# Kernel tuning notes

Hardware: AMD Instinct MI355X
Metric: run time of the kernel (lower is better)

## Reference

```python
import jax, jax.numpy as jnp
import numpy as np

IN_F, OUT_F, M, BATCH = 64, 64, 20, 1024


def setup_inputs() -> dict:
    key = jax.random.key(0)
    k1, k2 = jax.random.split(key)
    x = jax.random.normal(k1, (BATCH, IN_F), dtype=jnp.float32)
    # parameters, initialized as in the torch module
    z = jnp.tile(jnp.linspace(-1.5, 1.5, M, dtype=jnp.float32).reshape(1, 1, M), (OUT_F, IN_F, 1))
    q_mu = jax.random.normal(k2, (OUT_F, IN_F, M), dtype=jnp.float32) * 0.05
    q_log_var = jnp.full((OUT_F, IN_F, M), -3.0, dtype=jnp.float32)
    log_scale = jnp.zeros((OUT_F, IN_F), dtype=jnp.float32)
    log_variance = jnp.full((OUT_F, IN_F), -1.0, dtype=jnp.float32)
    return {"x": x, "z": z, "q_mu": q_mu, "q_log_var": q_log_var,
            "log_scale": log_scale, "log_variance": log_variance}


def reference(x, z, q_mu, q_log_var, log_scale, log_variance):
    """SVGP-KAN layer, RBF kernel, deterministic input path (x_var = 1e-6).

    Per edge (o,i): basis-function GP f(x) = sum_m w_m k(x, z_m),
    w_m ~ N(q_mu, q_var), k(x,z) = sig2 * exp(-(x-z)^2 / (2 l^2)).
    Gaussian input x ~ N(mu, v) -> closed-form moments (Psi statistics).
    """
    x_mean = x
    x_var = jnp.full_like(x, 1e-6)

    q_var = jnp.clip(jnp.exp(q_log_var), 1e-5)          # [O,I,M]
    sig2 = jnp.clip(jnp.exp(log_variance), 1e-5)        # [O,I]
    ell = jnp.clip(jnp.exp(log_scale), 0.1)             # [O,I] (rbf min_scale=0.1)

    # broadcast: batch x out x in x inducing
    xm = x_mean[:, None, :, None]                       # [B,1,I,1]
    xv = x_var[:, None, :, None]                        # [B,1,I,1]
    zz = z[None]                                        # [1,O,I,M]
    l2 = (ell * ell)[None, :, :, None]                  # [1,O,I,1]
    s2 = sig2[None, :, :, None]                         # [1,O,I,1]

    d2 = (xm - zz) ** 2                                 # [B,O,I,M]
    den1 = l2 + xv
    psi1 = s2 * jnp.sqrt(l2 / den1) * jnp.exp(-d2 / (2.0 * den1))  # E[k(x,z_m)]
    den2 = l2 + 2.0 * xv
    ek2 = (s2 * s2) * jnp.sqrt(l2 / den2) * jnp.exp(-d2 / den2)     # E[k(x,z_m)^2]

    qm = q_mu[None]                                     # [1,O,I,M]
    qv = q_var[None]
    edge_mean = jnp.sum(psi1 * qm, axis=-1)             # [B,O,I]
    edge_var = jnp.sum(ek2 * (qm * qm + qv) - psi1 * psi1 * (qm * qm), axis=-1)
    edge_var = jnp.clip(edge_var, 0.0)                  # [B,O,I]

    y_mean = edge_mean.sum(axis=2)                      # [B,O]
    y_var = edge_var.sum(axis=2)                        # [B,O]
    return y_mean, y_var
```

## Files before the change

kernel.cpp:

```cpp
#include <hip/hip_runtime.h>
#include <hip/hip_bf16.h>

#define OUT_F 64
#define IN_F 64
#define M_PTS 20
#define BATCH 1024

#if __has_builtin(__builtin_amdgcn_exp2f)
#define EXP2(x) __builtin_amdgcn_exp2f(x)
#else
#define EXP2(x) exp2f(x)
#endif

__device__ unsigned g_cp[OUT_F * M_PTS * IN_F];
__device__ float4   g_aux[OUT_F * IN_F];

static __device__ __forceinline__ unsigned f2bf(float f) {
    union { float f; unsigned u; } v; v.f = f;
    unsigned r = v.u + 0x7fffu + ((v.u >> 16) & 1u);
    return r >> 16;
}
static __device__ __forceinline__ float bflo(unsigned p) {
    union { unsigned u; float f; } v; v.u = p << 16; return v.f;
}
static __device__ __forceinline__ float bfhi(unsigned p) {
    union { unsigned u; float f; } v; v.u = p & 0xffff0000u; return v.f;
}

__global__ __launch_bounds__(256) void prep_kernel(
    const float* __restrict__ z, const float* __restrict__ q_mu,
    const float* __restrict__ q_log_var, const float* __restrict__ log_scale,
    const float* __restrict__ log_variance)
{
    int idx = blockIdx.x * 256 + threadIdx.x;
    if (idx >= OUT_F * M_PTS * IN_F) return;
    int i  = idx & 63;
    int om = idx >> 6;
    int m  = om % M_PTS;
    int o  = om / M_PTS;
    int e  = o * IN_F + i;
    int ge = e * M_PTS + m;

    const float LOG2E = 1.4426950408889634f;
    float ell  = fmaxf(expf(log_scale[e]), 0.1f);
    float l2   = ell * ell;
    float sig2 = fmaxf(expf(log_variance[e]), 1e-5f);
    float den1 = l2 + 1e-6f;
    float den2 = l2 + 2e-6f;
    float c1   = sig2 * sqrtf(l2 / den1);
    float c2   = sig2 * sig2 * sqrtf(l2 / den2);
    float s    = sqrtf(0.5f * LOG2E / den1);

    float qm  = q_mu[ge];
    float qv  = fmaxf(expf(q_log_var[ge]), 1e-5f);
    float qmc = c1 * qm;
    float A   = c2 * (qm * qm + qv);
    float B   = A - qmc * qmc;

    g_cp[idx] = f2bf(qmc) | (f2bf(B) << 16);
    if (m == 0) {
        float z0  = z[ge];
        float z19 = z[e * M_PTS + (M_PTS - 1)];
        float delta = (z19 - z0) * (1.0f / (M_PTS - 1));
        float sd = s * delta;
        g_aux[e] = make_float4(s, s * z0, 2.0f * sd, -(sd * sd));
    }
}

__global__ __launch_bounds__(256, 8) void gpkan_main(
    const float* __restrict__ x, float* __restrict__ out)
{
    __shared__ float  xs_lds[8 * 64];
    __shared__ float2 red[4][8][66];

    const int tid  = threadIdx.x;
    const int lane = tid & 63;
    const int wv   = __builtin_amdgcn_readfirstlane(tid >> 6);
    const int o    = blockIdx.y * 4 + wv;
    const int bc   = blockIdx.x;

    if (tid < 128)
        reinterpret_cast<float4*>(xs_lds)[tid] =
            reinterpret_cast<const float4*>(x + bc * 8 * IN_F)[tid];

    float4 aux = g_aux[(o << 6) + lane];
    const float s = aux.x, sz0 = aux.y, cu1 = aux.z, cu0 = aux.w;
    const float v = EXP2(cu0 + cu0);

    unsigned cp[M_PTS];
    #pragma unroll
    for (int m = 0; m < M_PTS; ++m)
        cp[m] = g_cp[((o * M_PTS + m) << 6) + lane];

    __syncthreads();

    #pragma unroll 1
    for (int p = 0; p < 4; ++p) {
        float xb0 = xs_lds[(p << 7) + lane];
        float xb1 = xs_lds[(p << 7) + 64 + lane];
        float dx0 = fmaf(s, xb0, -sz0);
        float dx1 = fmaf(s, xb1, -sz0);
        float t0  = EXP2(-(dx0 * dx0));
        float t1  = EXP2(-(dx1 * dx1));
        float ua0 = fminf(fmaf(cu1, dx0, cu0), 60.0f);
        float ua1 = fminf(fmaf(cu1, dx1, cu0), 60.0f);
        float w0  = EXP2(ua0);
        float w1  = EXP2(ua1);

        float em0 = 0.0f, em1 = 0.0f, ev0 = 0.0f, ev1 = 0.0f;
        #pragma unroll
        for (int m = 0; m < M_PTS; ++m) {
            unsigned c = cp[m];
            float qmc = bflo(c);
            float B   = bfhi(c);
            em0 = fmaf(qmc, t0, em0);
            em1 = fmaf(qmc, t1, em1);
            ev0 = fmaf(B, t0 * t0, ev0);
            ev1 = fmaf(B, t1 * t1, ev1);
            if (m < M_PTS - 1) { t0 *= w0; t1 *= w1; w0 *= v; w1 *= v; }
        }
        red[wv][2 * p + 0][lane] = make_float2(em0, fmaxf(ev0, 0.0f));
        red[wv][2 * p + 1][lane] = make_float2(em1, fmaxf(ev1, 0.0f));
    }
    __syncthreads();

    const int seg = lane >> 3, b8r = lane & 7;
    const float4* rp = reinterpret_cast<const float4*>(&red[wv][b8r][seg << 3]);
    float sm = 0.0f, sv = 0.0f;
    #pragma unroll
    for (int j = 0; j < 4; ++j) {
        float4 q = rp[j];
        sm += q.x + q.z;
        sv += q.y + q.w;
    }
    sm += __shfl_xor(sm, 8);  sv += __shfl_xor(sv, 8);
    sm += __shfl_xor(sm, 16); sv += __shfl_xor(sv, 16);
    sm += __shfl_xor(sm, 32); sv += __shfl_xor(sv, 32);

    if (lane < 8) {
        int b = (bc << 3) + lane;
        out[(b << 6) + o] = sm;
        out[(BATCH << 6) + (b << 6) + o] = sv;
    }
}

extern "C" void kernel_launch(void* const* d_in, const int* in_sizes, int n_in,
                              void* d_out, int out_size, void* d_ws, size_t ws_size,
                              hipStream_t stream) {
    const float* x            = (const float*)d_in[0];
    const float* z            = (const float*)d_in[1];
    const float* q_mu         = (const float*)d_in[2];
    const float* q_log_var    = (const float*)d_in[3];
    const float* log_scale    = (const float*)d_in[4];
    const float* log_variance = (const float*)d_in[5];
    float* out = (float*)d_out;

    prep_kernel<<<(OUT_F * M_PTS * IN_F + 255) / 256, 256, 0, stream>>>(
        z, q_mu, q_log_var, log_scale, log_variance);
    gpkan_main<<<dim3(BATCH / 8, OUT_F / 4), 256, 0, stream>>>(x, out);
}
```

Before: 21.99 us.

## Use single-wave blocks with shuffle-based transpose reduction instead of LDS

Changes the main kernel from 256-thread blocks (4 waves sharing an LDS-staged x tile) to 64-thread single-wave blocks that read x directly from global memory. The LDS reduction buffer and both __syncthreads are replaced by a recursive-halving shuffle reduction that sums 16 values across lanes. The batch loop is fully unrolled through a macro. The aim is to drop barrier and LDS overhead and expose more ILP. The cost is more blocks, redundant global x loads per wave, and higher register pressure from the unrolled body.

Measured after the change: 22.88 us. +4.1%, slower.

```diff
diff --git a/kernel.cpp b/kernel.cpp
--- a/kernel.cpp
+++ b/kernel.cpp
@@ -67,21 +67,41 @@
     }
 }
 
-__global__ __launch_bounds__(256, 8) void gpkan_main(
+#define BODY(P)                                                              \
+    {                                                                        \
+        float xb0 = xg[((2 * (P)) << 6) + lane];                             \
+        float xb1 = xg[((2 * (P) + 1) << 6) + lane];                         \
+        float dx0 = fmaf(s, xb0, -sz0);                                      \
+        float dx1 = fmaf(s, xb1, -sz0);                                      \
+        float t0  = EXP2(-(dx0 * dx0));                                      \
+        float t1  = EXP2(-(dx1 * dx1));                                      \
+        float w0  = EXP2(fminf(fmaf(cu1, dx0, cu0), 60.0f));                 \
+        float w1  = EXP2(fminf(fmaf(cu1, dx1, cu0), 60.0f));                 \
+        float em0 = 0.0f, em1 = 0.0f, ev0 = 0.0f, ev1 = 0.0f;                \
+        _Pragma("unroll")                                                    \
+        for (int m = 0; m < M_PTS; ++m) {                                    \
+            unsigned c = cp[m];                                              \
+            float qmc = bflo(c);                                             \
+            float B   = bfhi(c);                                             \
+            em0 = fmaf(qmc, t0, em0);                                        \
+            em1 = fmaf(qmc, t1, em1);                                        \
+            ev0 = fmaf(B, t0 * t0, ev0);                                     \
+            ev1 = fmaf(B, t1 * t1, ev1);                                     \
+            if (m < M_PTS - 1) { t0 *= w0; t1 *= w1; w0 *= v; w1 *= v; }     \
+        }                                                                    \
+        qa[2 * (P)]     = em0;                                               \
+        qa[2 * (P) + 1] = em1;                                               \
+        qa[8 + 2 * (P)] = fmaxf(ev0, 0.0f);                                  \
+        qa[9 + 2 * (P)] = fmaxf(ev1, 0.0f);                                  \
+    }
+
+__global__ __launch_bounds__(64, 8) void gpkan_main(
     const float* __restrict__ x, float* __restrict__ out)
 {
-    __shared__ float  xs_lds[8 * 64];
-    __shared__ float2 red[4][8][66];
-
-    const int tid  = threadIdx.x;
-    const int lane = tid & 63;
-    const int wv   = __builtin_amdgcn_readfirstlane(tid >> 6);
-    const int o    = blockIdx.y * 4 + wv;
-    const int bc   = blockIdx.x;
-
-    if (tid < 128)
-        reinterpret_cast<float4*>(xs_lds)[tid] =
-            reinterpret_cast<const float4*>(x + bc * 8 * IN_F)[tid];
+    const int blk  = blockIdx.x;
+    const int o    = blk >> 7;
+    const int bc   = blk & 127;
+    const int lane = threadIdx.x;
 
     float4 aux = g_aux[(o << 6) + lane];
     const float s = aux.x, sz0 = aux.y, cu1 = aux.z, cu0 = aux.w;
@@ -92,55 +112,51 @@
     for (int m = 0; m < M_PTS; ++m)
         cp[m] = g_cp[((o * M_PTS + m) << 6) + lane];
 
-    __syncthreads();
+    const float* __restrict__ xg = x + (bc << 9);
 
-    #pragma unroll 1
-    for (int p = 0; p < 4; ++p) {
-        float xb0 = xs_lds[(p << 7) + lane];
-        float xb1 = xs_lds[(p << 7) + 64 + lane];
-        float dx0 = fmaf(s, xb0, -sz0);
-        float dx1 = fmaf(s, xb1, -sz0);
-        float t0  = EXP2(-(dx0 * dx0));
-        float t1  = EXP2(-(dx1 * dx1));
-        float ua0 = fminf(fmaf(cu1, dx0, cu0), 60.0f);
-        float ua1 = fminf(fmaf(cu1, dx1, cu0), 60.0f);
-        float w0  = EXP2(ua0);
-        float w1  = EXP2(ua1);
+    float qa[16];
+    BODY(0) BODY(1) BODY(2) BODY(3)
 
-        float em0 = 0.0f, em1 = 0.0f, ev0 = 0.0f, ev1 = 0.0f;
-        #pragma unroll
-        for (int m = 0; m < M_PTS; ++m) {
-            unsigned c = cp[m];
-            float qmc = bflo(c);
-            float B   = bfhi(c);
-            em0 = fmaf(qmc, t0, em0);
-            em1 = fmaf(qmc, t1, em1);
-            ev0 = fmaf(B, t0 * t0, ev0);
-            ev1 = fmaf(B, t1 * t1, ev1);
-            if (m < M_PTS - 1) { t0 *= w0; t1 *= w1; w0 *= v; w1 *= v; }
-        }
-        red[wv][2 * p + 0][lane] = make_float2(em0, fmaxf(ev0, 0.0f));
-        red[wv][2 * p + 1][lane] = make_float2(em1, fmaxf(ev1, 0.0f));
+    const bool s5 = (lane & 32) != 0;
+    const bool s4 = (lane & 16) != 0;
+    const bool s3 = (lane & 8) != 0;
+    const bool s2 = (lane & 4) != 0;
+
+    float k8[8];
+    #pragma unroll
+    for (int j = 0; j < 8; ++j) {
+        float keep = s5 ? qa[j + 8] : qa[j];
+        float send = s5 ? qa[j] : qa[j + 8];
+        k8[j] = keep + __shfl_xor(send, 32);
     }
-    __syncthreads();
-
-    const int seg = lane >> 3, b8r = lane & 7;
-    const float4* rp = reinterpret_cast<const float4*>(&red[wv][b8r][seg << 3]);
-    float sm = 0.0f, sv = 0.0f;
+    float k4[4];
     #pragma unroll
     for (int j = 0; j < 4; ++j) {
-        float4 q = rp[j];
-        sm += q.x + q.z;
-        sv += q.y + q.w;
+        float keep = s4 ? k8[j + 4] : k8[j];
+        float send = s4 ? k8[j] : k8[j + 4];
+        k4[j] = keep + __shfl_xor(send, 16);
     }
-    sm += __shfl_xor(sm, 8);  sv += __shfl_xor(sv, 8);
-    sm += __shfl_xor(sm, 16); sv += __shfl_xor(sv, 16);
-    sm += __shfl_xor(sm, 32); sv += __shfl_xor(sv, 32);
+    float k2[2];
+    #pragma unroll
+    for (int j = 0; j < 2; ++j) {
+        float keep = s3 ? k4[j + 2] : k4[j];
+        float send = s3 ? k4[j] : k4[j + 2];
+        k2[j] = keep + __shfl_xor(send, 8);
+    }
+    float k1;
+    {
+        float keep = s2 ? k2[1] : k2[0];
+        float send = s2 ? k2[0] : k2[1];
+        k1 = keep + __shfl_xor(send, 4);
+    }
+    k1 += __shfl_xor(k1, 2);
+    k1 += __shfl_xor(k1, 1);
 
-    if (lane < 8) {
-        int b = (bc << 3) + lane;
-        out[(b << 6) + o] = sm;
-        out[(BATCH << 6) + (b << 6) + o] = sv;
+    if ((lane & 3) == 0) {
+        int row   = ((lane >> 4) & 1) * 4 + ((lane >> 3) & 1) * 2 + ((lane >> 2) & 1);
+        int is_ev = (lane >> 5) & 1;
+        int b     = (bc << 3) + row;
+        out[is_ev * (BATCH * OUT_F) + b * OUT_F + o] = k1;
     }
 }
 
@@ -157,5 +173,5 @@
 
     prep_kernel<<<(OUT_F * M_PTS * IN_F + 255) / 256, 256, 0, stream>>>(
         z, q_mu, q_log_var, log_scale, log_variance);
-    gpkan_main<<<dim3(BATCH / 8, OUT_F / 4), 256, 0, stream>>>(x, out);
+    gpkan_main<<<128 * OUT_F, 64, 0, stream>>>(x, out);
 }
```
